# Optimization experiments

Measured on AMD Instinct MI355X. Metric: run time of the kernel, lower is better.

The kernel has to match this reference:

```python
import jax, jax.numpy as jnp
import numpy as np

B, N, C = 8, 4096, 768
H = 8            # num_heads (hardcoded in module)
D = C // H       # head_dim = 96


def setup_inputs() -> dict:
    key = jax.random.key(0)
    ks = jax.random.split(key, 10)
    s = 0.02
    return {
        "x_rgb": jax.random.normal(ks[0], (B, N, C), dtype=jnp.float32),
        "x_depth": jax.random.normal(ks[1], (B, N, C), dtype=jnp.float32),
        "W_qkv_rgb": jax.random.normal(ks[2], (3 * C, C), dtype=jnp.float32) * s,
        "b_qkv_rgb": jnp.zeros((3 * C,), dtype=jnp.float32),
        "W_qkv_depth": jax.random.normal(ks[3], (2 * C, C), dtype=jnp.float32) * s,
        "b_qkv_depth": jnp.zeros((2 * C,), dtype=jnp.float32),
        "W_out": jax.random.normal(ks[4], (C, C), dtype=jnp.float32) * s,
        "b_out": jnp.zeros((C,), dtype=jnp.float32),
        "adaptive_weights": jnp.ones((2,), dtype=jnp.float32),
    }


def reference(x_rgb, x_depth, W_qkv_rgb, b_qkv_rgb, W_qkv_depth, b_qkv_depth,
              W_out, b_out, adaptive_weights):
    scale = 1.0 / (D ** 0.5)
    # qkv projections (torch Linear: x @ W.T + b)
    qkv_rgb = (x_rgb @ W_qkv_rgb.T + b_qkv_rgb).reshape(B, N, 3, H, D)
    q_rgb, k_rgb, v_rgb = qkv_rgb[:, :, 0], qkv_rgb[:, :, 1], qkv_rgb[:, :, 2]
    kv_depth = (x_depth @ W_qkv_depth.T + b_qkv_depth).reshape(B, N, 2, H, D)
    k_depth, v_depth = kv_depth[:, :, 0], kv_depth[:, :, 1]

    # per-token attention across the head axis: scores are [B,N,H,H]
    attn_rgb = jax.nn.softmax(
        jnp.einsum('bnqd,bnkd->bnqk', q_rgb, k_depth) * scale, axis=-1)
    attn_depth = jax.nn.softmax(
        jnp.einsum('bnqd,bnkd->bnqk', q_rgb, k_rgb) * scale, axis=-1)

    # NOTE: faithful to original einsum with independent labels k and v:
    # sums over k (softmax -> 1) and over v independently.
    wv_rgb = jnp.einsum('bnqk,bnvd->bnqd', attn_rgb, v_depth)
    wv_depth = jnp.einsum('bnqk,bnvd->bnqd', attn_depth, v_rgb)

    w = jax.nn.sigmoid(adaptive_weights)
    x_fusion = (w[0] * wv_rgb + w[1] * wv_depth).reshape(B, N, C)
    x_fusion = x_fusion @ W_out.T + b_out
    return (x_rgb, x_fusion)
```

## Files before the change

### kernel.cpp

```cpp
#include <hip/hip_runtime.h>

typedef unsigned short u16;
typedef __attribute__((ext_vector_type(8))) short bf16x8;
typedef __attribute__((ext_vector_type(4))) float f32x4;

#define M_TOT 32768

__device__ __forceinline__ u16 f2b(float x) {
    union { float f; unsigned u; } c; c.f = x;
    unsigned r = c.u + 0x7fffu + ((c.u >> 16) & 1u);
    return (u16)(r >> 16);
}

__global__ void prep_b1(const float* __restrict__ Wr, const float* __restrict__ Wd,
                        const float* __restrict__ br, const float* __restrict__ bd,
                        const float* __restrict__ aw,
                        u16* __restrict__ B1, float* __restrict__ fb) {
    int id = blockIdx.x * 256 + threadIdx.x;
    if (id >= 96 * 1536) return;
    int d = id / 1536, k = id - d * 1536;
    float w0 = 1.f / (1.f + __expf(-aw[0]));
    float w1 = 1.f / (1.f + __expf(-aw[1]));
    float s = 0.f, v;
    if (k < 768) {
        for (int h = 0; h < 8; h++) s += Wr[(size_t)(1536 + h * 96 + d) * 768 + k];
        v = w1 * s;
    } else {
        for (int h = 0; h < 8; h++) s += Wd[(size_t)(768 + h * 96 + d) * 768 + (k - 768)];
        v = w0 * s;
    }
    B1[id] = f2b(v);
    if (k == 0) {
        float t = 0.f;
        for (int h = 0; h < 8; h++)
            t += w1 * br[1536 + h * 96 + d] + w0 * bd[768 + h * 96 + d];
        fb[d] = t;
    }
}

__global__ void prep_weff(const float* __restrict__ Wo, u16* __restrict__ Weff) {
    int id = blockIdx.x * 256 + threadIdx.x;
    if (id >= 768 * 96) return;
    int c = id / 96, d = id - c * 96;
    float s = 0.f;
    for (int h = 0; h < 8; h++) s += Wo[(size_t)c * 768 + h * 96 + d];
    Weff[id] = f2b(s);
}

__global__ __launch_bounds__(256) void gemm_f(const float* __restrict__ Xr,
                                              const float* __restrict__ Xd,
                                              const u16* __restrict__ B1,
                                              const float* __restrict__ fb,
                                              float* __restrict__ out0,
                                              u16* __restrict__ fbuf) {
    const int tid = threadIdx.x;
    const int lane = tid & 63;
    const int wv = (blockIdx.x << 2) | (tid >> 6);
    const int fr = lane & 15;
    const int fk = (lane >> 4) << 3;
    const size_t arow = (size_t)((wv << 4) | fr) * 768 + fk;

    const float* __restrict__ pr = Xr + arow;
    const float* __restrict__ pd = Xd + arow;
    float* __restrict__ po = out0 + arow;
    const u16* __restrict__ pb = B1 + fr * 1536 + fk;

    f32x4 acc[6] = {};

    float4 a0 = *(const float4*)(pr);
    float4 a1 = *(const float4*)(pr + 4);
    float4 a2 = *(const float4*)(pr + 32);
    float4 a3 = *(const float4*)(pr + 36);

    for (int ks = 0; ks < 24; ks++) {
        const int k0 = ks * 64;

        const float* pn = (ks >= 23) ? pr
                        : ((ks + 1 < 12) ? (pr + k0 + 64) : (pd + k0 - 704));
        float4 n0 = *(const float4*)(pn);
        float4 n1 = *(const float4*)(pn + 4);
        float4 n2 = *(const float4*)(pn + 32);
        float4 n3 = *(const float4*)(pn + 36);

        if (ks < 12) {
            *(float4*)(po + k0)      = a0;
            *(float4*)(po + k0 + 4)  = a1;
            *(float4*)(po + k0 + 32) = a2;
            *(float4*)(po + k0 + 36) = a3;
        }

        bf16x8 ab0, ab1;
        ab0[0] = (short)f2b(a0.x); ab0[1] = (short)f2b(a0.y);
        ab0[2] = (short)f2b(a0.z); ab0[3] = (short)f2b(a0.w);
        ab0[4] = (short)f2b(a1.x); ab0[5] = (short)f2b(a1.y);
        ab0[6] = (short)f2b(a1.z); ab0[7] = (short)f2b(a1.w);
        ab1[0] = (short)f2b(a2.x); ab1[1] = (short)f2b(a2.y);
        ab1[2] = (short)f2b(a2.z); ab1[3] = (short)f2b(a2.w);
        ab1[4] = (short)f2b(a3.x); ab1[5] = (short)f2b(a3.y);
        ab1[6] = (short)f2b(a3.z); ab1[7] = (short)f2b(a3.w);

        const u16* pbk = pb + k0;
#pragma unroll
        for (int j = 0; j < 6; j++)
            acc[j] = __builtin_amdgcn_mfma_f32_16x16x32_bf16(
                ab0, *(const bf16x8*)(pbk + j * 24576), acc[j], 0, 0, 0);
#pragma unroll
        for (int j = 0; j < 6; j++)
            acc[j] = __builtin_amdgcn_mfma_f32_16x16x32_bf16(
                ab1, *(const bf16x8*)(pbk + j * 24576 + 32), acc[j], 0, 0, 0);

        a0 = n0; a1 = n1; a2 = n2; a3 = n3;
    }

    const int em = (lane >> 4) << 2, en = lane & 15;
    const int orow = (wv << 4) + em;
#pragma unroll
    for (int j = 0; j < 6; j++) {
        const int dcol = j * 16 + en;
        const float bias = fb[dcol];
#pragma unroll
        for (int r = 0; r < 4; r++)
            fbuf[(size_t)(orow + r) * 96 + dcol] = f2b(acc[j][r] + bias);
    }
}

__global__ __launch_bounds__(256) void gemm_o(const u16* __restrict__ fbuf,
                                              const u16* __restrict__ Weff,
                                              const float* __restrict__ bout,
                                              float* __restrict__ out1) {
    const int tid = threadIdx.x;
    const int lane = tid & 63;
    const int wv = (blockIdx.x << 2) | (tid >> 6);
    const int mg = wv >> 3;
    const int nc = (wv & 7) * 96;
    const int fr = lane & 15, fk = (lane >> 4) << 3;

    const u16* pa = fbuf + (size_t)((mg << 4) | fr) * 96 + fk;
    bf16x8 A0 = *(const bf16x8*)(pa);
    bf16x8 A1 = *(const bf16x8*)(pa + 32);
    bf16x8 A2 = *(const bf16x8*)(pa + 64);

    const u16* pb = Weff + (size_t)(nc + fr) * 96 + fk;
    f32x4 acc[6] = {};
#pragma unroll
    for (int j = 0; j < 6; j++) {
        const u16* pbj = pb + j * 1536;
        acc[j] = __builtin_amdgcn_mfma_f32_16x16x32_bf16(
            A0, *(const bf16x8*)(pbj), acc[j], 0, 0, 0);
        acc[j] = __builtin_amdgcn_mfma_f32_16x16x32_bf16(
            A1, *(const bf16x8*)(pbj + 32), acc[j], 0, 0, 0);
        acc[j] = __builtin_amdgcn_mfma_f32_16x16x32_bf16(
            A2, *(const bf16x8*)(pbj + 64), acc[j], 0, 0, 0);
    }

    const int em = (lane >> 4) << 2, en = lane & 15;
    const int orow = (mg << 4) + em;
#pragma unroll
    for (int j = 0; j < 6; j++) {
        const int col = nc + j * 16 + en;
        const float bias = bout[col];
#pragma unroll
        for (int r = 0; r < 4; r++)
            out1[(size_t)(orow + r) * 768 + col] = acc[j][r] + bias;
    }
}

extern "C" void kernel_launch(void* const* d_in, const int* in_sizes, int n_in,
                              void* d_out, int out_size, void* d_ws, size_t ws_size,
                              hipStream_t stream) {
    const float* x_rgb       = (const float*)d_in[0];
    const float* x_depth     = (const float*)d_in[1];
    const float* W_qkv_rgb   = (const float*)d_in[2];
    const float* b_qkv_rgb   = (const float*)d_in[3];
    const float* W_qkv_depth = (const float*)d_in[4];
    const float* b_qkv_depth = (const float*)d_in[5];
    const float* W_out       = (const float*)d_in[6];
    const float* b_out       = (const float*)d_in[7];
    const float* aw          = (const float*)d_in[8];

    float* out0 = (float*)d_out;
    float* out1 = out0 + (size_t)M_TOT * 768;

    char* w = (char*)d_ws;
    u16*   B1   = (u16*)w;
    float* fb   = (float*)(w + 294912);
    u16*   Weff = (u16*)(w + 294912 + 512);
    u16*   fbuf = (u16*)(w + 294912 + 512 + 147456);

    prep_b1<<<576, 256, 0, stream>>>(W_qkv_rgb, W_qkv_depth, b_qkv_rgb, b_qkv_depth,
                                     aw, B1, fb);
    prep_weff<<<288, 256, 0, stream>>>(W_out, Weff);
    gemm_f<<<512, 256, 0, stream>>>(x_rgb, x_depth, B1, fb, out0, fbuf);
    gemm_o<<<4096, 256, 0, stream>>>(fbuf, Weff, b_out, out1);
}
```

Baseline: 443.6 us.

## Stage gemm_f A/B tiles through double-buffered LDS with coalesced loads

Restructures the fused projection GEMM so each block cooperatively loads a 64-row x 64-k slice of X and the B1 weight slice with coalesced float4/uint4 loads. It converts X to bf16 once into padded shared memory and double-buffers with barriers, prefetching two stages ahead in registers. Previously each wave read B1 fragments directly from global memory with strided per-lane loads. The aim is better global-load coalescing and overlap of memory with MFMA, at the cost of LDS usage and extra barriers in a kernel that is mostly bandwidth-bound on streaming X.

After: 404.6 us. 8.8% less time.

```diff
diff --git a/kernel.cpp b/kernel.cpp
--- a/kernel.cpp
+++ b/kernel.cpp
@@ -11,6 +11,11 @@
     unsigned r = c.u + 0x7fffu + ((c.u >> 16) & 1u);
     return (u16)(r >> 16);
 }
+
+#define BAR() do { __builtin_amdgcn_sched_barrier(0); \
+                   __builtin_amdgcn_s_barrier(); \
+                   __builtin_amdgcn_sched_barrier(0); } while (0)
+#define LGKM0() asm volatile("s_waitcnt lgkmcnt(0)" ::: "memory")
 
 __global__ void prep_b1(const float* __restrict__ Wr, const float* __restrict__ Wd,
                         const float* __restrict__ br, const float* __restrict__ bd,
@@ -47,80 +52,110 @@
     Weff[id] = f2b(s);
 }
 
+#define LDF 72
+
+__device__ __forceinline__ void stage_issue(const float* __restrict__ Xr,
+                                            const float* __restrict__ Xd,
+                                            const u16* __restrict__ B1,
+                                            int m0, int tid, int n,
+                                            float4 (&aF)[4], uint4 (&bF)[3]) {
+    const float* __restrict__ X = (n < 12) ? Xr : Xd;
+    const int kx = (n < 12) ? n * 64 : n * 64 - 768;
+#pragma unroll
+    for (int r = 0; r < 4; r++) {
+        int c = tid + 256 * r, row = c >> 4, colc = (c & 15) * 4;
+        aF[r] = *(const float4*)&X[(size_t)(m0 + row) * 768 + kx + colc];
+    }
+#pragma unroll
+    for (int r = 0; r < 3; r++) {
+        int c = tid + 256 * r, row = c >> 3, colc = (c & 7) * 8;
+        bF[r] = *(const uint4*)&B1[(size_t)row * 1536 + n * 64 + colc];
+    }
+}
+
+__device__ __forceinline__ void stage_commit(float* __restrict__ out0,
+                                             int m0, int tid, int n,
+                                             const float4 (&aF)[4], const uint4 (&bF)[3],
+                                             u16* __restrict__ sAb, u16* __restrict__ sBb) {
+#pragma unroll
+    for (int r = 0; r < 4; r++) {
+        int c = tid + 256 * r, row = c >> 4, colc = (c & 15) * 4;
+        if (n < 12)
+            *(float4*)&out0[(size_t)(m0 + row) * 768 + n * 64 + colc] = aF[r];
+        ushort4 bv;
+        bv.x = f2b(aF[r].x); bv.y = f2b(aF[r].y);
+        bv.z = f2b(aF[r].z); bv.w = f2b(aF[r].w);
+        *(ushort4*)&sAb[row * LDF + colc] = bv;
+    }
+#pragma unroll
+    for (int r = 0; r < 3; r++) {
+        int c = tid + 256 * r, row = c >> 3, colc = (c & 7) * 8;
+        *(uint4*)&sBb[row * LDF + colc] = bF[r];
+    }
+}
+
+__device__ __forceinline__ void mfma_tile(const u16* __restrict__ sAb,
+                                          const u16* __restrict__ sBb,
+                                          int wave, int fr, int fk, f32x4 (&acc)[6]) {
+#pragma unroll
+    for (int s = 0; s < 2; s++) {
+        bf16x8 a = *(const bf16x8*)&sAb[(wave * 16 + fr) * LDF + s * 32 + fk];
+#pragma unroll
+        for (int j = 0; j < 6; j++) {
+            bf16x8 b = *(const bf16x8*)&sBb[(j * 16 + fr) * LDF + s * 32 + fk];
+            acc[j] = __builtin_amdgcn_mfma_f32_16x16x32_bf16(a, b, acc[j], 0, 0, 0);
+        }
+    }
+}
+
 __global__ __launch_bounds__(256) void gemm_f(const float* __restrict__ Xr,
                                               const float* __restrict__ Xd,
                                               const u16* __restrict__ B1,
                                               const float* __restrict__ fb,
                                               float* __restrict__ out0,
                                               u16* __restrict__ fbuf) {
+    __shared__ u16 sA[2][64 * LDF];
+    __shared__ u16 sB[2][96 * LDF];
     const int tid = threadIdx.x;
-    const int lane = tid & 63;
-    const int wv = (blockIdx.x << 2) | (tid >> 6);
-    const int fr = lane & 15;
-    const int fk = (lane >> 4) << 3;
-    const size_t arow = (size_t)((wv << 4) | fr) * 768 + fk;
-
-    const float* __restrict__ pr = Xr + arow;
-    const float* __restrict__ pd = Xd + arow;
-    float* __restrict__ po = out0 + arow;
-    const u16* __restrict__ pb = B1 + fr * 1536 + fk;
+    const int m0 = blockIdx.x * 64;
+    const int lane = tid & 63, wave = tid >> 6;
+    const int fr = lane & 15, fk = (lane >> 4) * 8;
 
     f32x4 acc[6] = {};
-
-    float4 a0 = *(const float4*)(pr);
-    float4 a1 = *(const float4*)(pr + 4);
-    float4 a2 = *(const float4*)(pr + 32);
-    float4 a3 = *(const float4*)(pr + 36);
-
-    for (int ks = 0; ks < 24; ks++) {
-        const int k0 = ks * 64;
-
-        const float* pn = (ks >= 23) ? pr
-                        : ((ks + 1 < 12) ? (pr + k0 + 64) : (pd + k0 - 704));
-        float4 n0 = *(const float4*)(pn);
-        float4 n1 = *(const float4*)(pn + 4);
-        float4 n2 = *(const float4*)(pn + 32);
-        float4 n3 = *(const float4*)(pn + 36);
-
-        if (ks < 12) {
-            *(float4*)(po + k0)      = a0;
-            *(float4*)(po + k0 + 4)  = a1;
-            *(float4*)(po + k0 + 32) = a2;
-            *(float4*)(po + k0 + 36) = a3;
+    float4 a0[4], a1[4];
+    uint4  b0[3], b1[3];
+
+    stage_issue(Xr, Xd, B1, m0, tid, 0, a0, b0);
+    stage_issue(Xr, Xd, B1, m0, tid, 1, a1, b1);
+    stage_commit(out0, m0, tid, 0, a0, b0, &sA[0][0], &sB[0][0]);
+    LGKM0(); BAR();
+
+    for (int t = 0; t < 24; t += 2) {
+        if (t + 2 < 24) stage_issue(Xr, Xd, B1, m0, tid, t + 2, a0, b0);
+        mfma_tile(&sA[0][0], &sB[0][0], wave, fr, fk, acc);
+        BAR();
+        stage_commit(out0, m0, tid, t + 1, a1, b1, &sA[1][0], &sB[1][0]);
+        LGKM0(); BAR();
+
+        if (t + 3 < 24) stage_issue(Xr, Xd, B1, m0, tid, t + 3, a1, b1);
+        mfma_tile(&sA[1][0], &sB[1][0], wave, fr, fk, acc);
+        if (t + 2 < 24) {
+            BAR();
+            stage_commit(out0, m0, tid, t + 2, a0, b0, &sA[0][0], &sB[0][0]);
+            LGKM0(); BAR();
         }
-
-        bf16x8 ab0, ab1;
-        ab0[0] = (short)f2b(a0.x); ab0[1] = (short)f2b(a0.y);
-        ab0[2] = (short)f2b(a0.z); ab0[3] = (short)f2b(a0.w);
-        ab0[4] = (short)f2b(a1.x); ab0[5] = (short)f2b(a1.y);
-        ab0[6] = (short)f2b(a1.z); ab0[7] = (short)f2b(a1.w);
-        ab1[0] = (short)f2b(a2.x); ab1[1] = (short)f2b(a2.y);
-        ab1[2] = (short)f2b(a2.z); ab1[3] = (short)f2b(a2.w);
-        ab1[4] = (short)f2b(a3.x); ab1[5] = (short)f2b(a3.y);
-        ab1[6] = (short)f2b(a3.z); ab1[7] = (short)f2b(a3.w);
-
-        const u16* pbk = pb + k0;
-#pragma unroll
-        for (int j = 0; j < 6; j++)
-            acc[j] = __builtin_amdgcn_mfma_f32_16x16x32_bf16(
-                ab0, *(const bf16x8*)(pbk + j * 24576), acc[j], 0, 0, 0);
-#pragma unroll
-        for (int j = 0; j < 6; j++)
-            acc[j] = __builtin_amdgcn_mfma_f32_16x16x32_bf16(
-                ab1, *(const bf16x8*)(pbk + j * 24576 + 32), acc[j], 0, 0, 0);
-
-        a0 = n0; a1 = n1; a2 = n2; a3 = n3;
-    }
-
-    const int em = (lane >> 4) << 2, en = lane & 15;
-    const int orow = (wv << 4) + em;
+    }
+
+    const int em = (lane >> 4) * 4, en = lane & 15;
 #pragma unroll
     for (int j = 0; j < 6; j++) {
-        const int dcol = j * 16 + en;
-        const float bias = fb[dcol];
-#pragma unroll
-        for (int r = 0; r < 4; r++)
-            fbuf[(size_t)(orow + r) * 96 + dcol] = f2b(acc[j][r] + bias);
+        int dcol = j * 16 + en;
+        float bias = fb[dcol];
+#pragma unroll
+        for (int r = 0; r < 4; r++) {
+            int row = m0 + wave * 16 + em + r;
+            fbuf[(size_t)row * 96 + dcol] = f2b(acc[j][r] + bias);
+        }
     }
 }
 
```

## Split gemm_f K dimension across four waves with LDS reduction

Applied to the files above, without the earlier changes.

gemm_f now gives each block 16 rows instead of 64 and splits the 1536-long K loop across its four waves, two on the rgb half and two on the depth half. Partial accumulators are reduced through shared memory before the bias is added and the bf16 result written. This launches four times as many blocks and gives each wave a shorter, fully unrolled loop with B fragments loaded ahead, aiming for more memory-level parallelism on a bandwidth-bound pass. The cost is extra LDS traffic, a block barrier, and more registers for the prefetched B fragments.

After: 435.3 us. About the same (-1.9%).

```diff
diff --git a/kernel.cpp b/kernel.cpp
--- a/kernel.cpp
+++ b/kernel.cpp
@@ -47,80 +47,96 @@
     Weff[id] = f2b(s);
 }
 
-__global__ __launch_bounds__(256) void gemm_f(const float* __restrict__ Xr,
-                                              const float* __restrict__ Xd,
-                                              const u16* __restrict__ B1,
-                                              const float* __restrict__ fb,
-                                              float* __restrict__ out0,
-                                              u16* __restrict__ fbuf) {
+__global__ __launch_bounds__(256, 4) void gemm_f(const float* __restrict__ Xr,
+                                                 const float* __restrict__ Xd,
+                                                 const u16* __restrict__ B1,
+                                                 const float* __restrict__ fb,
+                                                 float* __restrict__ out0,
+                                                 u16* __restrict__ fbuf) {
+    __shared__ float red[4][16 * 96];
     const int tid = threadIdx.x;
-    const int lane = tid & 63;
-    const int wv = (blockIdx.x << 2) | (tid >> 6);
-    const int fr = lane & 15;
-    const int fk = (lane >> 4) << 3;
-    const size_t arow = (size_t)((wv << 4) | fr) * 768 + fk;
-
-    const float* __restrict__ pr = Xr + arow;
-    const float* __restrict__ pd = Xd + arow;
-    float* __restrict__ po = out0 + arow;
-    const u16* __restrict__ pb = B1 + fr * 1536 + fk;
+    const int lane = tid & 63, wave = tid >> 6;
+    const int m0 = blockIdx.x * 16;
+    const int fr = lane & 15, fk = (lane >> 4) * 8;
+
+    const bool isR = (wave < 2);
+    const int base = wave * 6;
+    const int kx = isR ? base * 64 : base * 64 - 768;
+    const float* __restrict__ X = isR ? Xr : Xd;
+
+    const float* __restrict__ pa = X + (size_t)(m0 + fr) * 768 + kx + fk;
+    float* __restrict__ po = out0 + (size_t)(m0 + fr) * 768 + base * 64 + fk;
+    const u16* __restrict__ pb = B1 + fr * 1536 + base * 64 + fk;
 
     f32x4 acc[6] = {};
 
-    float4 a0 = *(const float4*)(pr);
-    float4 a1 = *(const float4*)(pr + 4);
-    float4 a2 = *(const float4*)(pr + 32);
-    float4 a3 = *(const float4*)(pr + 36);
-
-    for (int ks = 0; ks < 24; ks++) {
-        const int k0 = ks * 64;
-
-        const float* pn = (ks >= 23) ? pr
-                        : ((ks + 1 < 12) ? (pr + k0 + 64) : (pd + k0 - 704));
-        float4 n0 = *(const float4*)(pn);
-        float4 n1 = *(const float4*)(pn + 4);
-        float4 n2 = *(const float4*)(pn + 32);
-        float4 n3 = *(const float4*)(pn + 36);
-
-        if (ks < 12) {
-            *(float4*)(po + k0)      = a0;
-            *(float4*)(po + k0 + 4)  = a1;
-            *(float4*)(po + k0 + 32) = a2;
-            *(float4*)(po + k0 + 36) = a3;
+    float4 c0 = *(const float4*)(pa);
+    float4 c1 = *(const float4*)(pa + 4);
+    float4 c2 = *(const float4*)(pa + 32);
+    float4 c3 = *(const float4*)(pa + 36);
+
+#pragma unroll
+    for (int i = 0; i < 6; i++) {
+        float4 n0, n1, n2, n3;
+        if (i < 5) {
+            const float* pn = pa + (i + 1) * 64;
+            n0 = *(const float4*)(pn);
+            n1 = *(const float4*)(pn + 4);
+            n2 = *(const float4*)(pn + 32);
+            n3 = *(const float4*)(pn + 36);
         }
 
+        if (isR) {
+            float* ps = po + i * 64;
+            *(float4*)(ps)      = c0;
+            *(float4*)(ps + 4)  = c1;
+            *(float4*)(ps + 32) = c2;
+            *(float4*)(ps + 36) = c3;
+        }
+
+        const u16* pbk = pb + i * 64;
+        bf16x8 b0[6], b1[6];
+#pragma unroll
+        for (int j = 0; j < 6; j++) {
+            b0[j] = *(const bf16x8*)(pbk + j * 24576);
+            b1[j] = *(const bf16x8*)(pbk + j * 24576 + 32);
+        }
+
         bf16x8 ab0, ab1;
-        ab0[0] = (short)f2b(a0.x); ab0[1] = (short)f2b(a0.y);
-        ab0[2] = (short)f2b(a0.z); ab0[3] = (short)f2b(a0.w);
-        ab0[4] = (short)f2b(a1.x); ab0[5] = (short)f2b(a1.y);
-        ab0[6] = (short)f2b(a1.z); ab0[7] = (short)f2b(a1.w);
-        ab1[0] = (short)f2b(a2.x); ab1[1] = (short)f2b(a2.y);
-        ab1[2] = (short)f2b(a2.z); ab1[3] = (short)f2b(a2.w);
-        ab1[4] = (short)f2b(a3.x); ab1[5] = (short)f2b(a3.y);
-        ab1[6] = (short)f2b(a3.z); ab1[7] = (short)f2b(a3.w);
-
-        const u16* pbk = pb + k0;
+        ab0[0] = (short)f2b(c0.x); ab0[1] = (short)f2b(c0.y);
+        ab0[2] = (short)f2b(c0.z); ab0[3] = (short)f2b(c0.w);
+        ab0[4] = (short)f2b(c1.x); ab0[5] = (short)f2b(c1.y);
+        ab0[6] = (short)f2b(c1.z); ab0[7] = (short)f2b(c1.w);
+        ab1[0] = (short)f2b(c2.x); ab1[1] = (short)f2b(c2.y);
+        ab1[2] = (short)f2b(c2.z); ab1[3] = (short)f2b(c2.w);
+        ab1[4] = (short)f2b(c3.x); ab1[5] = (short)f2b(c3.y);
+        ab1[6] = (short)f2b(c3.z); ab1[7] = (short)f2b(c3.w);
+
 #pragma unroll
         for (int j = 0; j < 6; j++)
-            acc[j] = __builtin_amdgcn_mfma_f32_16x16x32_bf16(
-                ab0, *(const bf16x8*)(pbk + j * 24576), acc[j], 0, 0, 0);
+            acc[j] = __builtin_amdgcn_mfma_f32_16x16x32_bf16(ab0, b0[j], acc[j], 0, 0, 0);
 #pragma unroll
         for (int j = 0; j < 6; j++)
-            acc[j] = __builtin_amdgcn_mfma_f32_16x16x32_bf16(
-                ab1, *(const bf16x8*)(pbk + j * 24576 + 32), acc[j], 0, 0, 0);
-
-        a0 = n0; a1 = n1; a2 = n2; a3 = n3;
-    }
-
-    const int em = (lane >> 4) << 2, en = lane & 15;
-    const int orow = (wv << 4) + em;
-#pragma unroll
-    for (int j = 0; j < 6; j++) {
-        const int dcol = j * 16 + en;
-        const float bias = fb[dcol];
+            acc[j] = __builtin_amdgcn_mfma_f32_16x16x32_bf16(ab1, b1[j], acc[j], 0, 0, 0);
+
+        c0 = n0; c1 = n1; c2 = n2; c3 = n3;
+    }
+
+    const int em = (lane >> 4) * 4, en = lane & 15;
+#pragma unroll
+    for (int j = 0; j < 6; j++)
 #pragma unroll
         for (int r = 0; r < 4; r++)
-            fbuf[(size_t)(orow + r) * 96 + dcol] = f2b(acc[j][r] + bias);
+            red[wave][(em + r) * 96 + j * 16 + en] = acc[j][r];
+
+    __syncthreads();
+
+#pragma unroll
+    for (int q = 0; q < 6; q++) {
+        const int e = q * 256 + tid;
+        const int col = e % 96;
+        float v = ((red[0][e] + red[1][e]) + red[2][e]) + red[3][e] + fb[col];
+        fbuf[(size_t)m0 * 96 + e] = f2b(v);
     }
 }
 
@@ -190,6 +206,6 @@
     prep_b1<<<576, 256, 0, stream>>>(W_qkv_rgb, W_qkv_depth, b_qkv_rgb, b_qkv_depth,
                                      aw, B1, fb);
     prep_weff<<<288, 256, 0, stream>>>(W_out, Weff);
-    gemm_f<<<512, 256, 0, stream>>>(x_rgb, x_depth, B1, fb, out0, fbuf);
+    gemm_f<<<2048, 256, 0, stream>>>(x_rgb, x_depth, B1, fb, out0, fbuf);
     gemm_o<<<4096, 256, 0, stream>>>(fbuf, Weff, b_out, out1);
 }
```

## Pre-swizzle B1 into MFMA fragment order, double-buffer B loads, merge prep kernels

Applied to the files above, without the earlier changes.

The B1 weight buffer is now written in MFMA-fragment order, so each lane reads contiguous 16-byte chunks laid out as lane*8. In gemm_f, both the A tile and all 12 B fragments for the next k-step are prefetched into registers, giving a double-buffered pipeline. The two prep kernels are merged into a single launch, removing one launch. The cost is much higher register pressure, with launch_bounds(256,2) and a fully unrolled 24-step loop, which could spill or lower occupancy.

Result: faster. 403.7 us (-9.0%).

```diff
diff --git a/kernel.cpp b/kernel.cpp
--- a/kernel.cpp
+++ b/kernel.cpp
@@ -12,104 +12,118 @@
     return (u16)(r >> 16);
 }
 
-__global__ void prep_b1(const float* __restrict__ Wr, const float* __restrict__ Wd,
-                        const float* __restrict__ br, const float* __restrict__ bd,
-                        const float* __restrict__ aw,
-                        u16* __restrict__ B1, float* __restrict__ fb) {
-    int id = blockIdx.x * 256 + threadIdx.x;
-    if (id >= 96 * 1536) return;
-    int d = id / 1536, k = id - d * 1536;
-    float w0 = 1.f / (1.f + __expf(-aw[0]));
-    float w1 = 1.f / (1.f + __expf(-aw[1]));
-    float s = 0.f, v;
-    if (k < 768) {
-        for (int h = 0; h < 8; h++) s += Wr[(size_t)(1536 + h * 96 + d) * 768 + k];
-        v = w1 * s;
+__global__ void prep(const float* __restrict__ Wr, const float* __restrict__ Wd,
+                     const float* __restrict__ br, const float* __restrict__ bd,
+                     const float* __restrict__ aw, const float* __restrict__ Wo,
+                     u16* __restrict__ B1p, float* __restrict__ fb,
+                     u16* __restrict__ Weff) {
+    if (blockIdx.x < 576) {
+        int id = blockIdx.x * 256 + threadIdx.x;
+        if (id >= 96 * 1536) return;
+        const int e = id & 7;
+        const int l = (id >> 3) & 63;
+        const int g = id >> 9;
+        const int q = g % 12, i = g / 12;
+        const int d = (q % 6) * 16 + (l & 15);
+        const int k = i * 64 + (q / 6) * 32 + ((l >> 4) << 3) + e;
+
+        float w0 = 1.f / (1.f + __expf(-aw[0]));
+        float w1 = 1.f / (1.f + __expf(-aw[1]));
+        float s = 0.f, v;
+        if (k < 768) {
+            for (int h = 0; h < 8; h++) s += Wr[(size_t)(1536 + h * 96 + d) * 768 + k];
+            v = w1 * s;
+        } else {
+            for (int h = 0; h < 8; h++) s += Wd[(size_t)(768 + h * 96 + d) * 768 + (k - 768)];
+            v = w0 * s;
+        }
+        B1p[id] = f2b(v);
+        if (k == 0) {
+            float t = 0.f;
+            for (int h = 0; h < 8; h++)
+                t += w1 * br[1536 + h * 96 + d] + w0 * bd[768 + h * 96 + d];
+            fb[d] = t;
+        }
     } else {
-        for (int h = 0; h < 8; h++) s += Wd[(size_t)(768 + h * 96 + d) * 768 + (k - 768)];
-        v = w0 * s;
-    }
-    B1[id] = f2b(v);
-    if (k == 0) {
-        float t = 0.f;
-        for (int h = 0; h < 8; h++)
-            t += w1 * br[1536 + h * 96 + d] + w0 * bd[768 + h * 96 + d];
-        fb[d] = t;
-    }
-}
-
-__global__ void prep_weff(const float* __restrict__ Wo, u16* __restrict__ Weff) {
-    int id = blockIdx.x * 256 + threadIdx.x;
-    if (id >= 768 * 96) return;
-    int c = id / 96, d = id - c * 96;
-    float s = 0.f;
-    for (int h = 0; h < 8; h++) s += Wo[(size_t)c * 768 + h * 96 + d];
-    Weff[id] = f2b(s);
-}
-
-__global__ __launch_bounds__(256) void gemm_f(const float* __restrict__ Xr,
-                                              const float* __restrict__ Xd,
-                                              const u16* __restrict__ B1,
-                                              const float* __restrict__ fb,
-                                              float* __restrict__ out0,
-                                              u16* __restrict__ fbuf) {
+        int id = (blockIdx.x - 576) * 256 + threadIdx.x;
+        if (id >= 768 * 96) return;
+        int c = id / 96, d = id - c * 96;
+        float s = 0.f;
+        for (int h = 0; h < 8; h++) s += Wo[(size_t)c * 768 + h * 96 + d];
+        Weff[id] = f2b(s);
+    }
+}
+
+__global__ __launch_bounds__(256, 2) void gemm_f(const float* __restrict__ Xr,
+                                                 const float* __restrict__ Xd,
+                                                 const u16* __restrict__ B1p,
+                                                 const float* __restrict__ fb,
+                                                 float* __restrict__ out0,
+                                                 u16* __restrict__ fbuf) {
     const int tid = threadIdx.x;
     const int lane = tid & 63;
     const int wv = (blockIdx.x << 2) | (tid >> 6);
-    const int fr = lane & 15;
-    const int fk = (lane >> 4) << 3;
-    const size_t arow = (size_t)((wv << 4) | fr) * 768 + fk;
-
-    const float* __restrict__ pr = Xr + arow;
-    const float* __restrict__ pd = Xd + arow;
-    float* __restrict__ po = out0 + arow;
-    const u16* __restrict__ pb = B1 + fr * 1536 + fk;
+    const int fr = lane & 15, fkq = lane >> 4;
+    const size_t rowoff = (size_t)((wv << 4) | fr) * 768;
+
+    const float* __restrict__ pr = Xr + rowoff + fkq * 8;
+    const float* __restrict__ pd = Xd + rowoff + fkq * 8;
+    float* __restrict__ po = out0 + rowoff + fkq * 8;
+    const u16* __restrict__ pB = B1p + lane * 8;
 
     f32x4 acc[6] = {};
-
-    float4 a0 = *(const float4*)(pr);
-    float4 a1 = *(const float4*)(pr + 4);
-    float4 a2 = *(const float4*)(pr + 32);
-    float4 a3 = *(const float4*)(pr + 36);
-
-    for (int ks = 0; ks < 24; ks++) {
-        const int k0 = ks * 64;
-
-        const float* pn = (ks >= 23) ? pr
-                        : ((ks + 1 < 12) ? (pr + k0 + 64) : (pd + k0 - 704));
-        float4 n0 = *(const float4*)(pn);
-        float4 n1 = *(const float4*)(pn + 4);
-        float4 n2 = *(const float4*)(pn + 32);
-        float4 n3 = *(const float4*)(pn + 36);
-
-        if (ks < 12) {
-            *(float4*)(po + k0)      = a0;
-            *(float4*)(po + k0 + 4)  = a1;
-            *(float4*)(po + k0 + 32) = a2;
-            *(float4*)(po + k0 + 36) = a3;
+    float4 A[2][4];
+    bf16x8 Bf[2][12];
+
+    A[0][0] = *(const float4*)(pr);
+    A[0][1] = *(const float4*)(pr + 4);
+    A[0][2] = *(const float4*)(pr + 32);
+    A[0][3] = *(const float4*)(pr + 36);
+#pragma unroll
+    for (int q = 0; q < 12; q++)
+        Bf[0][q] = *(const bf16x8*)(pB + q * 512);
+
+#pragma unroll
+    for (int i = 0; i < 24; i++) {
+        const int cur = i & 1, nxt = cur ^ 1;
+
+        if (i < 23) {
+            const int n = i + 1;
+            const float* s = (n < 12) ? (pr + n * 64) : (pd + (n - 12) * 64);
+            A[nxt][0] = *(const float4*)(s);
+            A[nxt][1] = *(const float4*)(s + 4);
+            A[nxt][2] = *(const float4*)(s + 32);
+            A[nxt][3] = *(const float4*)(s + 36);
+            const u16* bb = pB + n * 6144;
+#pragma unroll
+            for (int q = 0; q < 12; q++)
+                Bf[nxt][q] = *(const bf16x8*)(bb + q * 512);
+        }
+
+        if (i < 12) {
+            float* ps = po + i * 64;
+            *(float4*)(ps)      = A[cur][0];
+            *(float4*)(ps + 4)  = A[cur][1];
+            *(float4*)(ps + 32) = A[cur][2];
+            *(float4*)(ps + 36) = A[cur][3];
         }
 
         bf16x8 ab0, ab1;
-        ab0[0] = (short)f2b(a0.x); ab0[1] = (short)f2b(a0.y);
-        ab0[2] = (short)f2b(a0.z); ab0[3] = (short)f2b(a0.w);
-        ab0[4] = (short)f2b(a1.x); ab0[5] = (short)f2b(a1.y);
-        ab0[6] = (short)f2b(a1.z); ab0[7] = (short)f2b(a1.w);
-        ab1[0] = (short)f2b(a2.x); ab1[1] = (short)f2b(a2.y);
-        ab1[2] = (short)f2b(a2.z); ab1[3] = (short)f2b(a2.w);
-        ab1[4] = (short)f2b(a3.x); ab1[5] = (short)f2b(a3.y);
-        ab1[6] = (short)f2b(a3.z); ab1[7] = (short)f2b(a3.w);
-
-        const u16* pbk = pb + k0;
+        ab0[0] = (short)f2b(A[cur][0].x); ab0[1] = (short)f2b(A[cur][0].y);
+        ab0[2] = (short)f2b(A[cur][0].z); ab0[3] = (short)f2b(A[cur][0].w);
+        ab0[4] = (short)f2b(A[cur][1].x); ab0[5] = (short)f2b(A[cur][1].y);
+        ab0[6] = (short)f2b(A[cur][1].z); ab0[7] = (short)f2b(A[cur][1].w);
+        ab1[0] = (short)f2b(A[cur][2].x); ab1[1] = (short)f2b(A[cur][2].y);
+        ab1[2] = (short)f2b(A[cur][2].z); ab1[3] = (short)f2b(A[cur][2].w);
+        ab1[4] = (short)f2b(A[cur][3].x); ab1[5] = (short)f2b(A[cur][3].y);
+        ab1[6] = (short)f2b(A[cur][3].z); ab1[7] = (short)f2b(A[cur][3].w);
+
 #pragma unroll
         for (int j = 0; j < 6; j++)
-            acc[j] = __builtin_amdgcn_mfma_f32_16x16x32_bf16(
-                ab0, *(const bf16x8*)(pbk + j * 24576), acc[j], 0, 0, 0);
+            acc[j] = __builtin_amdgcn_mfma_f32_16x16x32_bf16(ab0, Bf[cur][j], acc[j], 0, 0, 0);
 #pragma unroll
         for (int j = 0; j < 6; j++)
-            acc[j] = __builtin_amdgcn_mfma_f32_16x16x32_bf16(
-                ab1, *(const bf16x8*)(pbk + j * 24576 + 32), acc[j], 0, 0, 0);
-
-        a0 = n0; a1 = n1; a2 = n2; a3 = n3;
+            acc[j] = __builtin_amdgcn_mfma_f32_16x16x32_bf16(ab1, Bf[cur][6 + j], acc[j], 0, 0, 0);
     }
 
     const int em = (lane >> 4) << 2, en = lane & 15;
@@ -182,14 +196,13 @@
     float* out1 = out0 + (size_t)M_TOT * 768;
 
     char* w = (char*)d_ws;
-    u16*   B1   = (u16*)w;
+    u16*   B1p  = (u16*)w;
     float* fb   = (float*)(w + 294912);
     u16*   Weff = (u16*)(w + 294912 + 512);
     u16*   fbuf = (u16*)(w + 294912 + 512 + 147456);
 
-    prep_b1<<<576, 256, 0, stream>>>(W_qkv_rgb, W_qkv_depth, b_qkv_rgb, b_qkv_depth,
-                                     aw, B1, fb);
-    prep_weff<<<288, 256, 0, stream>>>(W_out, Weff);
-    gemm_f<<<512, 256, 0, stream>>>(x_rgb, x_depth, B1, fb, out0, fbuf);
+    prep<<<864, 256, 0, stream>>>(W_qkv_rgb, W_qkv_depth, b_qkv_rgb, b_qkv_depth,
+                                  aw, W_out, B1p, fb, Weff);
+    gemm_f<<<512, 256, 0, stream>>>(x_rgb, x_depth, B1p, fb, out0, fbuf);
     gemm_o<<<4096, 256, 0, stream>>>(fbuf, Weff, b_out, out1);
 }
```
